# Kernel tuning notes

Hardware: AMD Instinct MI355X
Metric: run time of the kernel (lower is better)

The kernel has to match this reference:

```python
import jax, jax.numpy as jnp
import numpy as np
from jax import lax

NUM_CLASSES = 2
IOU_THRESH = 0.5
SCORE_THRESH = 0.5
K_CAND = 512        # per-class candidate pool fed to greedy NMS
MAX_PER_CLASS = 100
MAX_TOTAL = 100


def setup_inputs() -> dict:
    key = jax.random.key(0)
    k1, k2, k3 = jax.random.split(key, 3)
    B = 64
    pred_s1 = jax.random.normal(k1, (B, 19, 19, 3, 5 + NUM_CLASSES), dtype=jnp.float32)
    pred_s2 = jax.random.normal(k2, (B, 38, 38, 3, 5 + NUM_CLASSES), dtype=jnp.float32)
    pred_s3 = jax.random.normal(k3, (B, 76, 76, 3, 5 + NUM_CLASSES), dtype=jnp.float32)
    # standard YOLOv3 anchors (pixels) normalized by input size 608
    anchors_px = np.array([[10, 13], [16, 30], [33, 23], [30, 61], [62, 45],
                           [59, 119], [116, 90], [156, 198], [373, 326]], np.float32)
    anchors = jnp.asarray(anchors_px / 608.0)
    return {"pred_s1": pred_s1, "pred_s2": pred_s2, "pred_s3": pred_s3, "anchors": anchors}


def _decode(pred, anch):
    # pred: [B, g, g, A, 5+C]; anch: [A, 2] normalized wh
    g = pred.shape[1]
    box_xy = jax.nn.sigmoid(pred[..., 0:2])
    box_wh = jnp.exp(pred[..., 2:4]) * anch          # broadcast [A,2]
    obj = jax.nn.sigmoid(pred[..., 4:5])
    cls = jax.nn.sigmoid(pred[..., 5:])
    gx, gy = jnp.meshgrid(jnp.arange(g), jnp.arange(g))   # 'xy' indexing, as tf.meshgrid
    grid = jnp.stack([gx, gy], axis=-1)[:, :, None, :].astype(pred.dtype)  # [g,g,1,2]
    xy = (box_xy + grid) / jnp.float32(g)
    x1y1 = xy - box_wh / 2.0
    x2y2 = x1y1 + box_wh                              # YoloNMS: wh + xy(top-left)
    boxes = jnp.concatenate([x1y1, x2y2], axis=-1)    # [B,g,g,A,4]
    scores = obj * cls                                # [B,g,g,A,C]
    B = pred.shape[0]
    return boxes.reshape(B, -1, 4), scores.reshape(B, -1, NUM_CLASSES)


def _pairwise_iou(b):
    # b: [K,4] in (x1,y1,x2,y2); returns [K,K]
    a = b[:, None, :]
    c = b[None, :, :]
    iw = jnp.clip(jnp.minimum(a[..., 2], c[..., 2]) - jnp.maximum(a[..., 0], c[..., 0]), 0.0)
    ih = jnp.clip(jnp.minimum(a[..., 3], c[..., 3]) - jnp.maximum(a[..., 1], c[..., 1]), 0.0)
    inter = iw * ih
    area = jnp.clip(b[:, 2] - b[:, 0], 0.0) * jnp.clip(b[:, 3] - b[:, 1], 0.0)
    union = area[:, None] + area[None, :] - inter
    return inter / jnp.maximum(union, 1e-9)


def _nms_one_class(boxes, scores):
    # boxes: [N,4], scores: [N] -> candidate boxes/scores/keep mask, each len K_CAND
    sc, idx = lax.top_k(scores, K_CAND)               # sorted descending
    bx = boxes[idx]
    iou = lax.stop_gradient(_pairwise_iou(bx))
    valid = sc > SCORE_THRESH
    def body(i, keep):
        suppressed = jnp.any(keep & (iou[i] > IOU_THRESH))
        return keep.at[i].set(valid[i] & ~suppressed)
    keep = lax.fori_loop(0, K_CAND, body, jnp.zeros((K_CAND,), jnp.bool_))
    keep = keep & (jnp.cumsum(keep) <= MAX_PER_CLASS)
    return bx, sc, keep


def _nms_one_image(boxes, scores):
    # boxes: [N,4], scores: [N,C]
    bk, sk, keep = jax.vmap(_nms_one_class, in_axes=(None, 1))(boxes, scores)  # [C,K,*]
    sm = jnp.where(keep, sk, -1.0)
    cls_ids = jnp.broadcast_to(jnp.arange(NUM_CLASSES)[:, None], (NUM_CLASSES, K_CAND))
    sf = sm.reshape(-1)
    bf = bk.reshape(-1, 4)
    cf = cls_ids.reshape(-1)
    ts, ti = lax.top_k(sf, MAX_TOTAL)
    kept = ts > 0.0
    out_boxes = jnp.where(kept[:, None], jnp.clip(bf[ti], 0.0, 1.0), 0.0)  # clip_boxes=True
    out_scores = jnp.where(kept, ts, 0.0)
    out_classes = jnp.where(kept, cf[ti].astype(jnp.float32), 0.0)
    return out_boxes, out_scores, out_classes, jnp.sum(kept).astype(jnp.int32)


def reference(pred_s1, pred_s2, pred_s3, anchors):
    # scale masks: grid19 -> anchors[6:9], grid38 -> anchors[3:6], grid76 -> anchors[0:3]
    b1, s1 = _decode(pred_s1, anchors[6:9])
    b2, s2 = _decode(pred_s2, anchors[3:6])
    b3, s3 = _decode(pred_s3, anchors[0:3])
    boxes = jnp.concatenate([b1, b2, b3], axis=1)     # [B,N,4]
    scores = jnp.concatenate([s1, s2, s3], axis=1)    # [B,N,C]
    return jax.vmap(_nms_one_image)(boxes, scores)
```

## Files before the change

### kernel.cpp

```cpp
#include <hip/hip_runtime.h>
#include <cstdint>
#include <cstddef>

#define NTOT   22743
#define N1     1083
#define N12    5415
#define BATCH  64
#define KCAND  512
#define NSEG   16
#define SEGLEN 1422
#define CAPS   384
#define CAP    4096
#define MAXPC  100
#define MAXTOT 100
#define KITER  6

__device__ __forceinline__ float sigmoidf(float x) { return 1.0f / (1.0f + expf(-x)); }
__device__ __forceinline__ int SK4(int j) { return j + ((j >> 6) << 2); }

__global__ __launch_bounds__(256) void score_filter_kernel(
    const float* __restrict__ p1, const float* __restrict__ p2,
    const float* __restrict__ p3, uint2* __restrict__ cand,
    uint32_t* __restrict__ counts)
{
  const int blk  = blockIdx.x;
  const int b    = blk >> 4;
  const int s    = blk & 15;
  const int tid  = threadIdx.x;
  const int lane = tid & 63;

  __shared__ uint2    lst[2][CAPS];
  __shared__ uint32_t lcnt[2];

  if (tid < 2) lcnt[tid] = 0u;
  __syncthreads();

  const int beg = s * SEGLEN;
  const int end = (beg + SEGLEN < NTOT) ? beg + SEGLEN : NTOT;

  float4 v[KITER];
  #pragma unroll
  for (int k = 0; k < KITER; ++k) {
    int i0 = beg + tid + k * 256;
    if (i0 < end) {
      const float* p; int local, per;
      if (i0 < N1)       { p = p1; local = i0;        per = 1083; }
      else if (i0 < N12) { p = p2; local = i0 - N1;   per = 4332; }
      else               { p = p3; local = i0 - N12;  per = 17328; }
      const float* q = p + ((size_t)b * per + local) * 7;
      v[k] = *(const float4*)(q + 3);
    } else {
      v[k] = make_float4(0.f, -1.f, 0.f, 0.f);
    }
  }

  #pragma unroll
  for (int k = 0; k < KITER; ++k) {
    int i0 = beg + tid + k * 256;
    float s0 = 0.f, s1 = 0.f;
    float q4 = v[k].y;
    if (q4 > 0.f) {
      float obj = sigmoidf(q4);
      s0 = obj * sigmoidf(v[k].z);
      s1 = obj * sigmoidf(v[k].w);
    }
    #pragma unroll
    for (int c = 0; c < 2; c++) {
      float sc = (c == 0) ? s0 : s1;
      bool pred = sc > 0.5f;
      unsigned long long m = __ballot(pred ? 1 : 0);
      if (m != 0ull) {
        int leader = (int)__ffsll(m) - 1;
        uint32_t base = 0u;
        if (lane == leader) base = atomicAdd(&lcnt[c], (uint32_t)__popcll(m));
        base = (uint32_t)__shfl((int)base, leader);
        if (pred) {
          uint32_t off = base + (uint32_t)__popcll(m & ((1ull << lane) - 1ull));
          if (off < CAPS) lst[c][off] = make_uint2(__float_as_uint(sc), (uint32_t)i0);
        }
      }
    }
  }
  __syncthreads();

  #pragma unroll
  for (int c = 0; c < 2; c++) {
    uint32_t cnt = lcnt[c]; if (cnt > CAPS) cnt = CAPS;
    uint2* dst = cand + ((size_t)((b * 2 + c) * NSEG + s)) * CAPS;
    for (uint32_t i = tid; i < cnt; i += 256) dst[i] = lst[c][i];
    if (tid == 0) counts[(b * 2 + c) * NSEG + s] = cnt;
  }
}

__device__ void decode_box(const float* __restrict__ p1, const float* __restrict__ p2,
                           const float* __restrict__ p3, const float* __restrict__ anch,
                           int b, int i, float bb[4])
{
  const float* p; int local, g, abase, per;
  if (i < N1)       { p = p1; local = i;       g = 19; abase = 6; per = 1083; }
  else if (i < N12) { p = p2; local = i - N1;  g = 38; abase = 3; per = 4332; }
  else              { p = p3; local = i - N12; g = 76; abase = 0; per = 17328; }
  const float* q = p + ((size_t)b * per + local) * 7;
  int a    = local % 3;
  int cell = local / 3;
  int col  = cell % g;
  int row  = cell / g;
  float aw = anch[(abase + a) * 2 + 0];
  float ah = anch[(abase + a) * 2 + 1];
  float x = (sigmoidf(q[0]) + (float)col) / (float)g;
  float y = (sigmoidf(q[1]) + (float)row) / (float)g;
  float w = expf(q[2]) * aw;
  float h = expf(q[3]) * ah;
  float x1 = x - w * 0.5f;
  float y1 = y - h * 0.5f;
  bb[0] = x1; bb[1] = y1; bb[2] = x1 + w; bb[3] = y1 + h;
}

__global__ __launch_bounds__(1024) void nms_kernel(
    const uint2* __restrict__ cand, const uint32_t* __restrict__ counts,
    const float* __restrict__ p1, const float* __restrict__ p2,
    const float* __restrict__ p3, const float* __restrict__ anch,
    float* __restrict__ selScore, float* __restrict__ selBox,
    int* __restrict__ selRank, int* __restrict__ selCount)
{
  const int bc   = blockIdx.x;
  const int b    = bc >> 1;
  const int tid  = threadIdx.x;
  const int lane = tid & 63;

  __shared__ __attribute__((aligned(16))) unsigned long long bord[CAP];
  __shared__ __attribute__((aligned(16))) float bx1[544];
  __shared__ __attribute__((aligned(16))) float by1[544];
  __shared__ __attribute__((aligned(16))) float bx2[544];
  __shared__ __attribute__((aligned(16))) float by2[544];
  __shared__ __attribute__((aligned(16))) float ar[544];
  __shared__ uint32_t           skey[512];
  __shared__ unsigned long long msk[128][9];
  __shared__ unsigned long long kword[8];
  __shared__ uint32_t           hist3[768];
  __shared__ uint32_t           svar[8];

  if (tid < 768) hist3[tid] = 0u;
  if (tid == 0) svar[5] = 0u;
  if (tid < 512) {
    skey[tid] = 0u; int p = SK4(tid);
    bx1[p] = 0.f; by1[p] = 0.f; bx2[p] = 0.f; by2[p] = 0.f; ar[p] = 0.f;
  }

  uint32_t pc[17];
  pc[0] = 0;
  #pragma unroll
  for (int t = 0; t < 16; ++t) {
    uint32_t c = counts[bc * NSEG + t];
    if (c > CAPS) c = CAPS;
    pc[t + 1] = pc[t] + c;
  }
  const int n = ((int)pc[16] < CAP) ? (int)pc[16] : CAP;
  const int limit = (n < KCAND) ? n : KCAND;

  unsigned long long v0, v1, v2, v3;
  auto loadc = [&](int i) -> unsigned long long {
    if (i >= n) return 0ull;
    uint32_t ps = 0; int s = 0;
    #pragma unroll
    for (int t = 1; t < 16; ++t) {
      bool ge = (uint32_t)i >= pc[t];
      s += (int)ge; ps = ge ? pc[t] : ps;
    }
    uint2 e = cand[(size_t)(bc * NSEG + s) * CAPS + (i - (int)ps)];
    return ((unsigned long long)e.x << 32) | (uint32_t)(~e.y);
  };
  v0 = loadc(tid); v1 = loadc(tid + 1024); v2 = loadc(tid + 2048); v3 = loadc(tid + 3072);
  __syncthreads();

  uint32_t* bcnt = hist3;
  uint32_t* boff = hist3 + 256;
  uint32_t* bpre = hist3 + 512;

  #define BKT(vv) ((uint32_t)(((vv) >> 47) & 255u))
  if (v0) atomicAdd(&bcnt[BKT(v0)], 1u);
  if (v1) atomicAdd(&bcnt[BKT(v1)], 1u);
  if (v2) atomicAdd(&bcnt[BKT(v2)], 1u);
  if (v3) atomicAdd(&bcnt[BKT(v3)], 1u);
  __syncthreads();

  if (tid < 64) {
    uint32_t h0 = bcnt[lane * 4 + 0], h1 = bcnt[lane * 4 + 1];
    uint32_t h2 = bcnt[lane * 4 + 2], h3 = bcnt[lane * 4 + 3];
    uint32_t s3 = h3, s2 = h2 + s3, s1 = h1 + s2, s0 = h0 + s1;
    uint32_t acc = s0;
    #pragma unroll
    for (int o = 1; o < 64; o <<= 1) {
      uint32_t vv = __shfl_down(acc, (unsigned)o);
      acc += (lane + o < 64) ? vv : 0u;
    }
    uint32_t above = acc - s0;
    bpre[lane * 4 + 0] = above + s1;
    bpre[lane * 4 + 1] = above + s2;
    bpre[lane * 4 + 2] = above + s3;
    bpre[lane * 4 + 3] = above;
  }
  __syncthreads();

  if (v0) bord[bpre[BKT(v0)] + atomicAdd(&boff[BKT(v0)], 1u)] = v0;
  if (v1) bord[bpre[BKT(v1)] + atomicAdd(&boff[BKT(v1)], 1u)] = v1;
  if (v2) bord[bpre[BKT(v2)] + atomicAdd(&boff[BKT(v2)], 1u)] = v2;
  if (v3) bord[bpre[BKT(v3)] + atomicAdd(&boff[BKT(v3)], 1u)] = v3;
  __syncthreads();

  auto rankdec = [&](unsigned long long e) {
    if (e == 0ull) return;
    const uint32_t B = BKT(e);
    const uint32_t lo = bpre[B], sz = bcnt[B];
    if ((int)lo < KCAND) {
      int rank = (int)lo;
      for (uint32_t j = lo; j < lo + sz; ++j) rank += (int)(bord[j] > e);
      if (rank < KCAND) {
        int idx = (int)(~(uint32_t)e);
        float bb[4];
        decode_box(p1, p2, p3, anch, b, idx, bb);
        int p = SK4(rank);
        bx1[p] = bb[0]; by1[p] = bb[1]; bx2[p] = bb[2]; by2[p] = bb[3];
        ar[p]  = fmaxf(bb[2] - bb[0], 0.f) * fmaxf(bb[3] - bb[1], 0.f);
        skey[rank] = (uint32_t)(e >> 32);
      }
    }
  };
  rankdec(v0); rankdec(v1); rankdec(v2); rankdec(v3);
  #undef BKT
  __syncthreads();

  unsigned long long Kw = 0ull;
  int kept = 0;
  const int r = tid & 127;
  const int w = tid >> 7;

  for (int ch = 0; ch < 4; ++ch) {
    const int base = ch * 128;
    int rows = limit - base; if (rows > 128) rows = 128;

    if (r < rows) {
      const int i = base + r;
      if (w <= (i >> 6)) {
        const int ip = SK4(i);
        const float x1i = bx1[ip], y1i = by1[ip], x2i = bx2[ip], y2i = by2[ip];
        const float ai = ar[ip];
        unsigned long long mrow = 0ull;
        #pragma unroll
        for (int m4 = 0; m4 < 16; ++m4) {
          const int j0 = (w << 6) + (m4 << 2);
          const int a  = j0 + (w << 2);
          float4 X1 = *(const float4*)&bx1[a];
          float4 Y1 = *(const float4*)&by1[a];
          float4 X2 = *(const float4*)&bx2[a];
          float4 Y2 = *(const float4*)&by2[a];
          float4 AR = *(const float4*)&ar[a];
          #define IOU_BIT(JX1,JY1,JX2,JY2,JAR,J)                              \
            { float iw = fminf(x2i,(JX2)) - fmaxf(x1i,(JX1));                 \
              float ih = fminf(y2i,(JY2)) - fmaxf(y1i,(JY1));                 \
              iw = fmaxf(iw,0.f); ih = fmaxf(ih,0.f);                        \
              float inter = iw*ih;                                            \
              float uni = fmaxf(ai + (JAR) - inter, 1e-9f);                   \
              if ((inter/uni > 0.5f) && ((J) < i))                            \
                mrow |= 1ull << ((J) & 63); }
          IOU_BIT(X1.x, Y1.x, X2.x, Y2.x, AR.x, j0 + 0)
          IOU_BIT(X1.y, Y1.y, X2.y, Y2.y, AR.y, j0 + 1)
          IOU_BIT(X1.z, Y1.z, X2.z, Y2.z, AR.z, j0 + 2)
          IOU_BIT(X1.w, Y1.w, X2.w, Y2.w, AR.w, j0 + 3)
          #undef IOU_BIT
        }
        msk[r][w] = mrow;
      } else {
        msk[r][w] = 0ull;
      }
    }
    __syncthreads();

    if (tid < 64) {
      bool stop = false;
      for (int g = 0; g < 8 && !stop; ++g) {
        int r0 = g * 16;
        if (r0 >= rows) break;
        unsigned long long wbuf[16];
        #pragma unroll
        for (int k2 = 0; k2 < 16; ++k2)
          wbuf[k2] = (lane < 8 && (r0 + k2) < rows) ? msk[r0 + k2][lane] : 0ull;
        #pragma unroll
        for (int k2 = 0; k2 < 16; ++k2) {
          if (!stop) {
            int rr = r0 + k2;
            if (rr >= rows) { stop = true; }
            else {
              int i = base + rr;
              bool ov = (Kw & wbuf[k2]) != 0ull;
              if (!__any(ov)) {
                if (lane == (i >> 6)) Kw |= 1ull << (i & 63);
                if (++kept >= MAXPC) stop = true;
              }
            }
          }
        }
      }
      if (lane == 0) svar[5] = (kept >= MAXPC || (base + (rows > 0 ? rows : 0)) >= limit) ? 1u : 0u;
    }
    __syncthreads();
    if (svar[5] != 0u) break;
  }

  if (tid < 8) kword[tid] = Kw;
  __syncthreads();

  if (tid < 512) {
    int rr = tid;
    int wr = rr >> 6;
    unsigned long long kw = kword[wr];
    if ((kw >> (rr & 63)) & 1ull) {
      uint32_t p = 0;
      for (int ww = 0; ww < wr; ++ww) p += (uint32_t)__popcll(kword[ww]);
      p += (uint32_t)__popcll(kw & ((1ull << (rr & 63)) - 1ull));
      selScore[bc * MAXPC + p] = __uint_as_float(skey[rr]);
      selRank[bc * MAXPC + p]  = rr;
      int rp = SK4(rr);
      float* o = &selBox[(size_t)(bc * MAXPC + p) * 4];
      o[0] = bx1[rp]; o[1] = by1[rp]; o[2] = bx2[rp]; o[3] = by2[rp];
    }
  }
  if (tid == 0) {
    uint32_t tot = 0;
    for (int ww = 0; ww < 8; ++ww) tot += (uint32_t)__popcll(kword[ww]);
    selCount[bc] = (int)tot;
  }
}

__global__ __launch_bounds__(256) void merge_kernel(
    const float* __restrict__ selScore, const float* __restrict__ selBox,
    const int* __restrict__ selRank, const int* __restrict__ selCount,
    float* __restrict__ out)
{
  const int b   = blockIdx.x;
  const int tid = threadIdx.x;
  __shared__ float    es[200];
  __shared__ uint32_t ek[200];
  __shared__ float    eb[200][4];
  const int c0  = selCount[b * 2 + 0];
  const int c1  = selCount[b * 2 + 1];
  const int tot = c0 + c1;

  if (tid < tot) {
    int cls  = (tid < c0) ? 0 : 1;
    int slot = (cls == 0) ? tid : (tid - c0);
    int src  = (b * 2 + cls) * MAXPC + slot;
    es[tid] = selScore[src];
    ek[tid] = (uint32_t)(cls * KCAND + selRank[src]);
    eb[tid][0] = selBox[(size_t)src * 4 + 0];
    eb[tid][1] = selBox[(size_t)src * 4 + 1];
    eb[tid][2] = selBox[(size_t)src * 4 + 2];
    eb[tid][3] = selBox[(size_t)src * 4 + 3];
  }
  __syncthreads();

  float* outBoxes  = out;
  float* outScores = out + (size_t)BATCH * MAXTOT * 4;
  float* outCls    = outScores + (size_t)BATCH * MAXTOT;
  float* outCnt    = outCls + (size_t)BATCH * MAXTOT;
  const int filled = (tot < MAXTOT) ? tot : MAXTOT;

  if (tid < tot) {
    float    s  = es[tid];
    uint32_t fk = ek[tid];
    int rank = 0;
    for (int j = 0; j < tot; j++)
      rank += (int)((es[j] > s) || (es[j] == s && ek[j] < fk));
    if (rank < MAXTOT) {
      outScores[b * MAXTOT + rank] = s;
      outCls[b * MAXTOT + rank]    = (float)(fk >> 9);
      float* ob = &outBoxes[(size_t)(b * MAXTOT + rank) * 4];
      ob[0] = fminf(fmaxf(eb[tid][0], 0.f), 1.f);
      ob[1] = fminf(fmaxf(eb[tid][1], 0.f), 1.f);
      ob[2] = fminf(fmaxf(eb[tid][2], 0.f), 1.f);
      ob[3] = fminf(fmaxf(eb[tid][3], 0.f), 1.f);
    }
  }
  if (tid >= filled && tid < MAXTOT) {
    outScores[b * MAXTOT + tid] = 0.f;
    outCls[b * MAXTOT + tid]    = 0.f;
    float* ob = &outBoxes[(size_t)(b * MAXTOT + tid) * 4];
    ob[0] = 0.f; ob[1] = 0.f; ob[2] = 0.f; ob[3] = 0.f;
  }
  if (tid == 0) outCnt[b] = (float)filled;
}

extern "C" void kernel_launch(void* const* d_in, const int* in_sizes, int n_in,
                              void* d_out, int out_size, void* d_ws, size_t ws_size,
                              hipStream_t stream)
{
  const float* p1   = (const float*)d_in[0];
  const float* p2   = (const float*)d_in[1];
  const float* p3   = (const float*)d_in[2];
  const float* anch = (const float*)d_in[3];

  uint8_t* ws = (uint8_t*)d_ws;
  uint32_t* counts = (uint32_t*)ws;
  uint2*    cand   = (uint2*)(ws + 16384);
  uint8_t*  wp     = ws + 16384 + (size_t)128 * NSEG * CAPS * 8;
  float*    selScore = (float*)wp;         wp += (size_t)BATCH * 2 * MAXPC * 4;
  float*    selBox   = (float*)wp;         wp += (size_t)BATCH * 2 * MAXPC * 16;
  int*      selRank  = (int*)wp;           wp += (size_t)BATCH * 2 * MAXPC * 4;
  int*      selCount = (int*)wp;

  score_filter_kernel<<<BATCH * NSEG, 256, 0, stream>>>(p1, p2, p3, cand, counts);
  nms_kernel<<<BATCH * 2, 1024, 0, stream>>>(cand, counts, p1, p2, p3, anch,
                                             selScore, selBox, selRank, selCount);
  merge_kernel<<<BATCH, 256, 0, stream>>>(selScore, selBox, selRank, selCount,
                                          (float*)d_out);
}
```

Measured before the change: 57.04 us.

## Decode candidate boxes in score filter and store packed keys with boxes

Box decoding moves from the NMS kernel into the score-filter kernel. Each surviving candidate's box is decoded there and written to a new float4 workspace array, and the sort key is prepacked into a 64-bit value. The NMS kernel then reads the precomputed box by candidate position instead of doing scattered global gathers plus sigmoid and exp per ranked candidate. In exchange it decodes every candidate above threshold (up to 384 per segment) rather than only the top 512, which adds extra global writes and shared memory in the filter kernel.

```diff
diff --git a/kernel.cpp b/kernel.cpp
--- a/kernel.cpp
+++ b/kernel.cpp
@@ -20,7 +20,8 @@
 
 __global__ __launch_bounds__(256) void score_filter_kernel(
     const float* __restrict__ p1, const float* __restrict__ p2,
-    const float* __restrict__ p3, uint2* __restrict__ cand,
+    const float* __restrict__ p3, const float* __restrict__ anch,
+    unsigned long long* __restrict__ candKV, float4* __restrict__ candBox,
     uint32_t* __restrict__ counts)
 {
   const int blk  = blockIdx.x;
@@ -29,8 +30,9 @@
   const int tid  = threadIdx.x;
   const int lane = tid & 63;
 
-  __shared__ uint2    lst[2][CAPS];
-  __shared__ uint32_t lcnt[2];
+  __shared__ unsigned long long lkv[2][CAPS];
+  __shared__ float4             lbox[2][CAPS];
+  __shared__ uint32_t           lcnt[2];
 
   if (tid < 2) lcnt[tid] = 0u;
   __syncthreads();
@@ -76,7 +78,30 @@
         base = (uint32_t)__shfl((int)base, leader);
         if (pred) {
           uint32_t off = base + (uint32_t)__popcll(m & ((1ull << lane) - 1ull));
-          if (off < CAPS) lst[c][off] = make_uint2(__float_as_uint(sc), (uint32_t)i0);
+          if (off < CAPS) {
+            lkv[c][off] = ((unsigned long long)__float_as_uint(sc) << 32)
+                          | (uint32_t)(~(uint32_t)i0);
+            const float* p; int local, per, g, abase;
+            if (i0 < N1)       { p = p1; local = i0;        per = 1083;  g = 19; abase = 6; }
+            else if (i0 < N12) { p = p2; local = i0 - N1;   per = 4332;  g = 38; abase = 3; }
+            else               { p = p3; local = i0 - N12;  per = 17328; g = 76; abase = 0; }
+            const float* q = p + ((size_t)b * per + local) * 7;
+            float q0 = q[0], q1v = q[1], q2v = q[2];
+            float q3v = v[k].x;
+            int a    = local % 3;
+            int cell = local / 3;
+            int col  = cell % g;
+            int row  = cell / g;
+            float aw = anch[(abase + a) * 2 + 0];
+            float ah = anch[(abase + a) * 2 + 1];
+            float x = (sigmoidf(q0)  + (float)col) / (float)g;
+            float y = (sigmoidf(q1v) + (float)row) / (float)g;
+            float w = expf(q2v) * aw;
+            float h = expf(q3v) * ah;
+            float x1 = x - w * 0.5f;
+            float y1 = y - h * 0.5f;
+            lbox[c][off] = make_float4(x1, y1, x1 + w, y1 + h);
+          }
         }
       }
     }
@@ -86,45 +111,20 @@
   #pragma unroll
   for (int c = 0; c < 2; c++) {
     uint32_t cnt = lcnt[c]; if (cnt > CAPS) cnt = CAPS;
-    uint2* dst = cand + ((size_t)((b * 2 + c) * NSEG + s)) * CAPS;
-    for (uint32_t i = tid; i < cnt; i += 256) dst[i] = lst[c][i];
+    unsigned long long* dk = candKV  + (size_t)((b * 2 + c) * NSEG + s) * CAPS;
+    float4*             db = candBox + (size_t)((b * 2 + c) * NSEG + s) * CAPS;
+    for (uint32_t i = tid; i < cnt; i += 256) { dk[i] = lkv[c][i]; db[i] = lbox[c][i]; }
     if (tid == 0) counts[(b * 2 + c) * NSEG + s] = cnt;
   }
 }
 
-__device__ void decode_box(const float* __restrict__ p1, const float* __restrict__ p2,
-                           const float* __restrict__ p3, const float* __restrict__ anch,
-                           int b, int i, float bb[4])
-{
-  const float* p; int local, g, abase, per;
-  if (i < N1)       { p = p1; local = i;       g = 19; abase = 6; per = 1083; }
-  else if (i < N12) { p = p2; local = i - N1;  g = 38; abase = 3; per = 4332; }
-  else              { p = p3; local = i - N12; g = 76; abase = 0; per = 17328; }
-  const float* q = p + ((size_t)b * per + local) * 7;
-  int a    = local % 3;
-  int cell = local / 3;
-  int col  = cell % g;
-  int row  = cell / g;
-  float aw = anch[(abase + a) * 2 + 0];
-  float ah = anch[(abase + a) * 2 + 1];
-  float x = (sigmoidf(q[0]) + (float)col) / (float)g;
-  float y = (sigmoidf(q[1]) + (float)row) / (float)g;
-  float w = expf(q[2]) * aw;
-  float h = expf(q[3]) * ah;
-  float x1 = x - w * 0.5f;
-  float y1 = y - h * 0.5f;
-  bb[0] = x1; bb[1] = y1; bb[2] = x1 + w; bb[3] = y1 + h;
-}
-
 __global__ __launch_bounds__(1024) void nms_kernel(
-    const uint2* __restrict__ cand, const uint32_t* __restrict__ counts,
-    const float* __restrict__ p1, const float* __restrict__ p2,
-    const float* __restrict__ p3, const float* __restrict__ anch,
+    const unsigned long long* __restrict__ candKV,
+    const float4* __restrict__ candBox, const uint32_t* __restrict__ counts,
     float* __restrict__ selScore, float* __restrict__ selBox,
     int* __restrict__ selRank, int* __restrict__ selCount)
 {
   const int bc   = blockIdx.x;
-  const int b    = bc >> 1;
   const int tid  = threadIdx.x;
   const int lane = tid & 63;
 
@@ -158,19 +158,22 @@
   const int n = ((int)pc[16] < CAP) ? (int)pc[16] : CAP;
   const int limit = (n < KCAND) ? n : KCAND;
 
-  unsigned long long v0, v1, v2, v3;
-  auto loadc = [&](int i) -> unsigned long long {
-    if (i >= n) return 0ull;
+  int pos0 = -1, pos1 = -1, pos2 = -1, pos3 = -1;
+  auto loadc = [&](int i, int& pos) -> unsigned long long {
+    if (i >= n) { pos = -1; return 0ull; }
     uint32_t ps = 0; int s = 0;
     #pragma unroll
     for (int t = 1; t < 16; ++t) {
       bool ge = (uint32_t)i >= pc[t];
       s += (int)ge; ps = ge ? pc[t] : ps;
     }
-    uint2 e = cand[(size_t)(bc * NSEG + s) * CAPS + (i - (int)ps)];
-    return ((unsigned long long)e.x << 32) | (uint32_t)(~e.y);
+    pos = (int)((size_t)(bc * NSEG + s) * CAPS + (i - (int)ps));
+    return candKV[pos];
   };
-  v0 = loadc(tid); v1 = loadc(tid + 1024); v2 = loadc(tid + 2048); v3 = loadc(tid + 3072);
+  unsigned long long v0 = loadc(tid, pos0);
+  unsigned long long v1 = loadc(tid + 1024, pos1);
+  unsigned long long v2 = loadc(tid + 2048, pos2);
+  unsigned long long v3 = loadc(tid + 3072, pos3);
   __syncthreads();
 
   uint32_t* bcnt = hist3;
@@ -208,7 +211,7 @@
   if (v3) bord[bpre[BKT(v3)] + atomicAdd(&boff[BKT(v3)], 1u)] = v3;
   __syncthreads();
 
-  auto rankdec = [&](unsigned long long e) {
+  auto rankdec = [&](unsigned long long e, int pos) {
     if (e == 0ull) return;
     const uint32_t B = BKT(e);
     const uint32_t lo = bpre[B], sz = bcnt[B];
@@ -216,17 +219,15 @@
       int rank = (int)lo;
       for (uint32_t j = lo; j < lo + sz; ++j) rank += (int)(bord[j] > e);
       if (rank < KCAND) {
-        int idx = (int)(~(uint32_t)e);
-        float bb[4];
-        decode_box(p1, p2, p3, anch, b, idx, bb);
+        float4 bb = candBox[pos];
         int p = SK4(rank);
-        bx1[p] = bb[0]; by1[p] = bb[1]; bx2[p] = bb[2]; by2[p] = bb[3];
-        ar[p]  = fmaxf(bb[2] - bb[0], 0.f) * fmaxf(bb[3] - bb[1], 0.f);
+        bx1[p] = bb.x; by1[p] = bb.y; bx2[p] = bb.z; by2[p] = bb.w;
+        ar[p]  = fmaxf(bb.z - bb.x, 0.f) * fmaxf(bb.w - bb.y, 0.f);
         skey[rank] = (uint32_t)(e >> 32);
       }
     }
   };
-  rankdec(v0); rankdec(v1); rankdec(v2); rankdec(v3);
+  rankdec(v0, pos0); rankdec(v1, pos1); rankdec(v2, pos2); rankdec(v3, pos3);
   #undef BKT
   __syncthreads();
 
@@ -400,16 +401,18 @@
   const float* anch = (const float*)d_in[3];
 
   uint8_t* ws = (uint8_t*)d_ws;
-  uint32_t* counts = (uint32_t*)ws;
-  uint2*    cand   = (uint2*)(ws + 16384);
-  uint8_t*  wp     = ws + 16384 + (size_t)128 * NSEG * CAPS * 8;
+  uint32_t*           counts  = (uint32_t*)ws;
+  unsigned long long* candKV  = (unsigned long long*)(ws + 16384);
+  float4*             candBox = (float4*)(ws + 16384 + (size_t)128 * NSEG * CAPS * 8);
+  uint8_t* wp = ws + 16384 + (size_t)128 * NSEG * CAPS * 8 + (size_t)128 * NSEG * CAPS * 16;
   float*    selScore = (float*)wp;         wp += (size_t)BATCH * 2 * MAXPC * 4;
   float*    selBox   = (float*)wp;         wp += (size_t)BATCH * 2 * MAXPC * 16;
   int*      selRank  = (int*)wp;           wp += (size_t)BATCH * 2 * MAXPC * 4;
   int*      selCount = (int*)wp;
 
-  score_filter_kernel<<<BATCH * NSEG, 256, 0, stream>>>(p1, p2, p3, cand, counts);
-  nms_kernel<<<BATCH * 2, 1024, 0, stream>>>(cand, counts, p1, p2, p3, anch,
+  score_filter_kernel<<<BATCH * NSEG, 256, 0, stream>>>(p1, p2, p3, anch,
+                                                        candKV, candBox, counts);
+  nms_kernel<<<BATCH * 2, 1024, 0, stream>>>(candKV, candBox, counts,
                                              selScore, selBox, selRank, selCount);
   merge_kernel<<<BATCH, 256, 0, stream>>>(selScore, selBox, selRank, selCount,
                                           (float*)d_out);
```

After: 67.27 us. +17.9%, slower.
